# Optimization experiments

Hardware: AMD Instinct MI355X
Metric: run time of the kernel (lower is better)

The kernel has to match this reference:

```python
import jax, jax.numpy as jnp
import numpy as np

NUM_ROUTE = 3

def squash(x, axis=-1):
    sn = jnp.sum(x * x, axis=axis, keepdims=True)
    return (sn / (1.0 + sn)) * x / (jnp.sqrt(sn) + 1e-8)

def setup_inputs() -> dict:
    key = jax.random.key(0)
    ks = jax.random.split(key, 10)
    B, T, N, D = 16, 12, 1024, 64
    E, ES, HS, HT = 16, 16, 16, 64
    TT = HS * T
    u = lambda k, sh: jax.random.uniform(k, sh, jnp.float32, -0.1, 0.1)
    return {
        "x": jax.random.normal(ks[0], (B, T, N, D), jnp.float32),
        "node_embeddings": jax.random.normal(ks[1], (N, E), jnp.float32),
        "time_eb": jax.random.normal(ks[2], (B, ES), jnp.float32),
        "teb": jax.random.normal(ks[3], (B, T, ES), jnp.float32),
        "W_p": u(ks[4], (D, D)),
        "b_p": u(ks[5], (D,)),
        "t_adj": u(ks[6], (ES, HT, TT)),
        "adj": u(ks[7], (ES, HS, N)),
        "weights_spa": u(ks[8], (E, D, D)),
        "bias_spa": u(ks[9], (E, D)),
    }

def reference(x, node_embeddings, time_eb, teb, W_p, b_p, t_adj, adj, weights_spa, bias_spa):
    B, T, N, D = x.shape
    HS = adj.shape[1]
    lrelu = lambda y: jax.nn.leaky_relu(y, 0.01)

    # primary capsules
    Pcaps_out = squash(x @ W_p.T + b_p)                      # [B,T,N,D]
    dadj = jnp.einsum('btd,dhn->bthn', teb, adj)             # [B,T,HS,N]
    test1 = jnp.einsum('bthn,btnd->bthd', jax.nn.softmax(dadj, axis=-2), Pcaps_out)

    # prediction tensor u_hat[b,t,h,n,d] = squash(test1)[b,t,h,d] * Pcaps_out[b,t,n,d]
    k_test = jax.lax.stop_gradient(Pcaps_out)
    u_hat = jax.lax.stop_gradient(squash(test1)[:, :, :, None, :] * Pcaps_out[:, :, None, :, :])

    # dynamic routing-by-agreement (detached, as in the torch code)
    b = jnp.zeros((B, T, HS, N), x.dtype)
    for _ in range(NUM_ROUTE):
        c = jax.nn.softmax(b, axis=2)
        v = squash(jnp.einsum('bthn,bthnd->bthd', c, u_hat))
        b = b + jnp.einsum('bthd,btnd->bthn', v, k_test)

    c = jax.nn.softmax(b + dadj, axis=2)                     # [B,T,HS,N]
    s = jnp.einsum('bthn,btnd->bthd', c, Pcaps_out)          # [B,T,HS,D]

    mask_template = jnp.linspace(1.0, float(T), T) / 12.0    # [T]
    hyper = (s + mask_template[None, :, None, None]).reshape(B, T * HS, D)

    dyn = jnp.einsum('bd,dhk->bhk', time_eb, t_adj)          # [B,HT,TT]
    tem = lrelu(jnp.einsum('bhk,bkd->bhd', dyn, hyper))      # [B,HT,D]
    ret = lrelu(jnp.einsum('bhk,bhd->bkd', dyn, tem)).reshape(B, T, HS, D) + s

    v2 = squash(ret)
    recon = jnp.einsum('bthn,bthd->btnd', c, v2)             # [B,T,N,D]

    w_sp = jnp.einsum('nd,dio->nio', node_embeddings, weights_spa)  # [N,D,D]
    b_sp = node_embeddings @ bias_spa                                # [N,D]
    out = jnp.einsum('btni,nio->btno', recon, w_sp) + b_sp
    return lrelu(out + x), jax.lax.stop_gradient(c), jax.lax.stop_gradient(dyn)
```

## Files before the change

### kernel.cpp

```cpp
#include <hip/hip_runtime.h>
#include <math.h>

#define B_ 16
#define T_ 12
#define N_ 1024
#define D_ 64
#define HS_ 16
#define HT_ 64
#define TT_ 192
#define BT_ 192

typedef _Float16 f16x2 __attribute__((ext_vector_type(2)));
typedef _Float16 f16x8v __attribute__((ext_vector_type(8)));
typedef float f32x4v __attribute__((ext_vector_type(4)));
typedef unsigned int u32x4v __attribute__((ext_vector_type(4)));

__device__ __forceinline__ unsigned int pkrtz(float a, float b){
    auto r = __builtin_amdgcn_cvt_pkrtz(a, b);
    return __builtin_bit_cast(unsigned int, r);
}
__device__ __forceinline__ float fdot2u(unsigned int a, unsigned int b, float c){
    return __builtin_amdgcn_fdot2(__builtin_bit_cast(f16x2, a),
                                  __builtin_bit_cast(f16x2, b), c, false);
}
__device__ __forceinline__ float loF(unsigned int a){ f16x2 h = __builtin_bit_cast(f16x2, a); return (float)h.x; }
__device__ __forceinline__ float hiF(unsigned int a){ f16x2 h = __builtin_bit_cast(f16x2, a); return (float)h.y; }

__device__ __forceinline__ float lrelu_(float v){ return v > 0.f ? v : 0.01f*v; }
__device__ __forceinline__ float squash_sc(float sn){ return (sn/(1.f+sn))/(sqrtf(sn)+1e-8f); }

__device__ __forceinline__ float wredsum64(float v){
    #pragma unroll
    for (int mk = 1; mk < 64; mk <<= 1) v += __shfl_xor(v, mk, 64);
    return v;
}

__global__ __launch_bounds__(256, 1) void k_P(const float* __restrict__ x,
        const float* __restrict__ Wp, const float* __restrict__ bp,
        unsigned int* __restrict__ Ppk){
    __shared__ unsigned int xst[128*36];
    int t = threadIdx.x, w = t >> 6, l = t & 63;
    int lr = l & 15, lk = l >> 4;
    size_t rbase = (size_t)blockIdx.x*1024 + blockIdx.y*128;
    const float* xb = x + rbase*64;
    #pragma unroll
    for (int j = 0; j < 16; ++j){
        int idx = j*256 + t;
        int row = idx >> 5, cp = idx & 31;
        float2 xv = *(const float2*)(xb + row*64 + 2*cp);
        xst[row*36 + cp] = pkrtz(xv.x, xv.y);
    }
    f16x8v bf[4][2];
    float bpv[4];
    #pragma unroll
    for (int nt = 0; nt < 4; ++nt){
        #pragma unroll
        for (int ks = 0; ks < 2; ++ks){
            const float* wr = Wp + (nt*16 + lr)*64 + ks*32 + lk*8;
            u32x4v bw;
            #pragma unroll
            for (int j = 0; j < 4; ++j){
                float2 w2 = *(const float2*)(wr + 2*j);
                bw[j] = pkrtz(w2.x, w2.y);
            }
            bf[nt][ks] = __builtin_bit_cast(f16x8v, bw);
        }
        bpv[nt] = bp[nt*16 + lr];
    }
    __syncthreads();

    #pragma unroll
    for (int mi = 0; mi < 2; ++mi){
        int mt = 2*w + mi;
        f32x4v acc0 = {0.f,0.f,0.f,0.f}, acc1 = {0.f,0.f,0.f,0.f};
        f32x4v acc2 = {0.f,0.f,0.f,0.f}, acc3 = {0.f,0.f,0.f,0.f};
        #pragma unroll
        for (int ks = 0; ks < 2; ++ks){
            u32x4v au = *(u32x4v*)&xst[(mt*16 + lr)*36 + ks*16 + lk*4];
            f16x8v af = __builtin_bit_cast(f16x8v, au);
            acc0 = __builtin_amdgcn_mfma_f32_16x16x32_f16(af, bf[0][ks], acc0, 0, 0, 0);
            acc1 = __builtin_amdgcn_mfma_f32_16x16x32_f16(af, bf[1][ks], acc1, 0, 0, 0);
            acc2 = __builtin_amdgcn_mfma_f32_16x16x32_f16(af, bf[2][ks], acc2, 0, 0, 0);
            acc3 = __builtin_amdgcn_mfma_f32_16x16x32_f16(af, bf[3][ks], acc3, 0, 0, 0);
        }
        #pragma unroll
        for (int i = 0; i < 4; ++i){
            int row = mt*16 + lk*4 + i;
            float y0 = acc0[i] + bpv[0];
            float y1 = acc1[i] + bpv[1];
            float y2 = acc2[i] + bpv[2];
            float y3 = acc3[i] + bpv[3];
            float p0 = __shfl_xor(y0, 1, 64);
            float p1 = __shfl_xor(y1, 1, 64);
            float p2 = __shfl_xor(y2, 1, 64);
            float p3 = __shfl_xor(y3, 1, 64);
            if (!(l & 1)){
                int cb = lr >> 1;
                xst[row*36 +      cb] = pkrtz(y0, p0);
                xst[row*36 +  8 + cb] = pkrtz(y1, p1);
                xst[row*36 + 16 + cb] = pkrtz(y2, p2);
                xst[row*36 + 24 + cb] = pkrtz(y3, p3);
            }
        }
    }
    __syncthreads();
    unsigned int* pb = Ppk + rbase*32;
    #pragma unroll
    for (int q = 0; q < 4; ++q){
        int idx4 = q*256 + t;
        int r2 = idx4 >> 3, jq = idx4 & 7;
        uint4 v;
        v.x = xst[r2*36 + 4*jq];   v.y = xst[r2*36 + 4*jq + 1];
        v.z = xst[r2*36 + 4*jq+2]; v.w = xst[r2*36 + 4*jq + 3];
        ((uint4*)pb)[idx4] = v;
    }
}

template<int MODE>
__global__ __launch_bounds__(256, 2) void kA(const unsigned int* __restrict__ Ppk,
        float* __restrict__ scb,
        const float* __restrict__ teb, const float* __restrict__ adj,
        float* __restrict__ dadjb,
        const float* __restrict__ tpIn, const float* __restrict__ spart,
        float* __restrict__ v1buf, const float* __restrict__ vsumIn,
        float* __restrict__ vsumOut,
        float* __restrict__ tpOut, float* __restrict__ spOut,
        float* __restrict__ cout){
    __shared__ unsigned int PL[128*36];
    __shared__ unsigned int vLp[16*36];
    __shared__ float bL[16*130];
    __shared__ float cL[128*20];
    __shared__ float scL[128];
    __shared__ float snH[2][128];
    int bt = blockIdx.x, ch = blockIdx.y;
    int t = threadIdx.x, w = t >> 6, l = t & 63;
    int n0 = ch*128;

    const uint4* Pg = (const uint4*)(Ppk + ((size_t)bt*1024 + n0)*32);
    #pragma unroll
    for (int k = 0; k < 4; ++k){
        int idx4 = t + 256*k;
        uint4 u = Pg[idx4];
        *(uint4*)&PL[(idx4 >> 3)*36 + 4*(idx4 & 7)] = u;
    }
    if (MODE != 0){
        if (t < 128) scL[t] = scb[(size_t)bt*1024 + n0 + t];
        float sp = 0.f;
        if (MODE == 1){
            #pragma unroll
            for (int c = 0; c < 8; ++c) sp += spart[((size_t)bt*8 + c)*64 + l];
            sp *= (1.f/16.f);
        }
        #pragma unroll
        for (int i = 0; i < 4; ++i){
            int h = 4*w + i;
            float s = 0.f;
            #pragma unroll
            for (int c = 0; c < 8; ++c)
                s += tpIn[(((size_t)bt*8 + c)*16 + h)*64 + l];
            size_t oi = ((size_t)bt*16 + h)*64 + l;
            float vs;
            if (MODE == 1){
                float sn = wredsum64(s*s);
                float v1 = s*squash_sc(sn);
                v1buf[oi] = v1;
                float q = v1*sp;
                float sn2 = wredsum64(q*q);
                vs = q*squash_sc(sn2);
            } else {
                float q = v1buf[oi]*s;
                float sn = wredsum64(q*q);
                vs = vsumIn[oi] + q*squash_sc(sn);
            }
            if (MODE != 3) vsumOut[oi] = vs;
            float vo = __shfl_xor(vs, 1, 64);
            if (!(l & 1)) vLp[h*36 + (l >> 1)] = pkrtz(vs, vo);
        }
    }
    __syncthreads();

    {
        int n = t & 127, hg = t >> 7;
        if (MODE == 0){
            float s = 0.f;
            #pragma unroll
            for (int j = 0; j < 4; ++j){
                uint4 pq = *(uint4*)&PL[n*36 + hg*16 + 4*j];
                s += loF(pq.x)*loF(pq.x) + hiF(pq.x)*hiF(pq.x);
                s += loF(pq.y)*loF(pq.y) + hiF(pq.y)*hiF(pq.y);
                s += loF(pq.z)*loF(pq.z) + hiF(pq.z)*hiF(pq.z);
                s += loF(pq.w)*loF(pq.w) + hiF(pq.w)*hiF(pq.w);
            }
            snH[hg][n] = s;
        }
        float acc8[8];
        #pragma unroll
        for (int i = 0; i < 8; ++i) acc8[i] = 0.f;
        if (MODE != 0){
            #pragma unroll
            for (int j = 0; j < 8; ++j){
                uint4 pq = *(uint4*)&PL[n*36 + 4*j];
                #pragma unroll
                for (int i = 0; i < 8; ++i){
                    uint4 vq = *(uint4*)&vLp[(hg*8 + i)*36 + 4*j];
                    acc8[i] = fdot2u(pq.x, vq.x, acc8[i]);
                    acc8[i] = fdot2u(pq.y, vq.y, acc8[i]);
                    acc8[i] = fdot2u(pq.z, vq.z, acc8[i]);
                    acc8[i] = fdot2u(pq.w, vq.w, acc8[i]);
                }
            }
            float scn = scL[n];
            #pragma unroll
            for (int i = 0; i < 8; ++i) acc8[i] *= scn;
        }
        if (MODE == 0){
            float tl[16];
            #pragma unroll
            for (int e = 0; e < 16; ++e) tl[e] = teb[bt*16 + e];
            #pragma unroll
            for (int i = 0; i < 8; ++i){
                int h = hg*8 + i;
                float s = 0.f;
                #pragma unroll
                for (int e = 0; e < 16; ++e)
                    s += tl[e]*adj[(((e << 4) + h) << 10) + n0 + n];
                acc8[i] = s;
                dadjb[((size_t)bt*16 + h)*1024 + n0 + n] = s;
            }
        }
        if (MODE == 3){
            #pragma unroll
            for (int i = 0; i < 8; ++i)
                acc8[i] += dadjb[((size_t)bt*16 + hg*8 + i)*1024 + n0 + n];
        }
        #pragma unroll
        for (int i = 0; i < 8; ++i) bL[(hg*8 + i)*130 + n] = acc8[i];
    }
    __syncthreads();

    if (t < 128){
        int n = t;
        float scn;
        if (MODE == 0){
            scn = squash_sc(snH[0][n] + snH[1][n]);
            scL[n] = scn;
            scb[(size_t)bt*1024 + n0 + n] = scn;
        } else {
            scn = scL[n];
        }
        float M = -1e30f;
        #pragma unroll
        for (int h = 0; h < 16; ++h) M = fmaxf(M, bL[h*130 + n]);
        float S = 0.f; float ev[16];
        #pragma unroll
        for (int h = 0; h < 16; ++h){ ev[h] = __expf(bL[h*130 + n] - M); S += ev[h]; }
        float inv = 1.f/S;
        #pragma unroll
        for (int h = 0; h < 16; ++h){
            float cv = ev[h]*inv;
            cL[n*20 + h] = cv*scn;
            if (MODE == 3) cout[((size_t)bt*16 + h)*1024 + n0 + n] = cv;
        }
    }
    __syncthreads();

    float acc[4] = {0.f,0.f,0.f,0.f};
    float sp2 = 0.f;
    #pragma unroll 2
    for (int n = 0; n < 128; ++n){
        unsigned int pv = PL[n*36 + (l >> 1)];
        float p = (l & 1) ? hiF(pv) : loF(pv);
        float4 c4 = *(float4*)&cL[n*20 + 4*w];
        acc[0] += c4.x*p; acc[1] += c4.y*p; acc[2] += c4.z*p; acc[3] += c4.w*p;
        if (MODE == 0) sp2 += scL[n]*p;
    }
    #pragma unroll
    for (int i = 0; i < 4; ++i)
        tpOut[(((size_t)bt*8 + ch)*16 + 4*w + i)*64 + l] = acc[i];
    if (MODE == 0 && w == 0)
        spOut[((size_t)bt*8 + ch)*64 + l] = sp2;
}

__global__ __launch_bounds__(256) void k_s(const float* __restrict__ tpart,
        float* __restrict__ sout){
    int bt = blockIdx.x;
    int w = threadIdx.x >> 6, l = threadIdx.x & 63;
    #pragma unroll
    for (int i = 0; i < 4; ++i){
        int h = 4*w + i;
        float s = 0.f;
        #pragma unroll
        for (int c = 0; c < 8; ++c)
            s += tpart[(((size_t)bt*8 + c)*16 + h)*64 + l];
        sout[((size_t)bt*16 + h)*64 + l] = s;
    }
}

__global__ __launch_bounds__(256) void k_wsp(const float* __restrict__ ne,
        const float* __restrict__ wspa, const float* __restrict__ bspa,
        unsigned int* __restrict__ wpkg, float* __restrict__ bspg){
    __shared__ float wspaL[16*512];
    __shared__ float neL[32*16];
    int ioc = blockIdx.x, nc = blockIdx.y;
    int t = threadIdx.x, w = t >> 6, o = t & 63;
    #pragma unroll
    for (int k = 0; k < 8; ++k){
        int idx4 = t + 256*k;
        int e = idx4 >> 7, j4 = idx4 & 127;
        *(float4*)&wspaL[e*512 + 4*j4] =
            *(const float4*)(wspa + (size_t)e*4096 + ioc*512 + 4*j4);
    }
    #pragma unroll
    for (int k = 0; k < 2; ++k)
        neL[k*256 + t] = ne[(size_t)nc*512 + k*256 + t];
    __syncthreads();
    int c0 = (2*w)*64 + o, c1 = (2*w+1)*64 + o;
    #pragma unroll 2
    for (int n = 0; n < 32; ++n){
        float a0 = 0.f, a1 = 0.f;
        #pragma unroll
        for (int e = 0; e < 16; ++e){
            float nv = neL[n*16 + e];
            a0 += nv*wspaL[e*512 + c0];
            a1 += nv*wspaL[e*512 + c1];
        }
        wpkg[((size_t)(nc*32 + n))*2048 + (ioc*4 + w)*64 + o] = pkrtz(a0, a1);
    }
    if (ioc == 0){
        #pragma unroll
        for (int k = 0; k < 8; ++k){
            int idx = k*256 + t;
            int n = idx >> 6, o2 = idx & 63;
            float a = 0.f;
            #pragma unroll
            for (int e = 0; e < 16; ++e)
                a += neL[n*16 + e]*bspa[e*64 + o2];
            bspg[(size_t)(nc*32 + n)*64 + o2] = a;
        }
    }
}

__global__ __launch_bounds__(256) void k_dyntem(const float* __restrict__ timeb,
        const float* __restrict__ tadj, const float* __restrict__ sbuf,
        float* __restrict__ dyn, float* __restrict__ tem){
    __shared__ float dynL[192];
    __shared__ float part[4][64];
    int b = blockIdx.x, h = blockIdx.y, t = threadIdx.x;
    if (t < 192){
        float a = 0.f;
        #pragma unroll
        for (int e = 0; e < 16; ++e)
            a += timeb[b*16 + e]*tadj[((size_t)e*HT_ + h)*TT_ + t];
        dynL[t] = a;
        dyn[((size_t)b*HT_ + h)*TT_ + t] = a;
    }
    __syncthreads();
    int p = t >> 6, d = t & 63;
    const float* sb = sbuf + (size_t)b*TT_*64;
    float a = 0.f;
    #pragma unroll 4
    for (int k = 48*p; k < 48*p + 48; ++k)
        a += dynL[k]*(sb[(size_t)k*64 + d] + (float)((k >> 4) + 1)*(1.f/12.f));
    part[p][d] = a;
    __syncthreads();
    if (t < 64)
        tem[((size_t)b*HT_ + h)*64 + t] =
            lrelu_(part[0][t] + part[1][t] + part[2][t] + part[3][t]);
}

__global__ __launch_bounds__(256) void k_retv2(const float* __restrict__ dyn,
        const float* __restrict__ temb, const float* __restrict__ sbuf,
        float* __restrict__ v2){
    int b = blockIdx.x, kg = blockIdx.y;
    int w = threadIdx.x >> 6, l = threadIdx.x & 63;
    int k = kg*4 + w;
    const float* tb = temb + (size_t)b*HT_*64;
    float a0 = 0.f, a1 = 0.f;
    #pragma unroll 4
    for (int h = 0; h < HT_; h += 2){
        a0 += dyn[((size_t)b*HT_ + h  )*TT_ + k] * tb[(size_t)h*64 + l];
        a1 += dyn[((size_t)b*HT_ + h+1)*TT_ + k] * tb[(size_t)(h+1)*64 + l];
    }
    float a = lrelu_(a0 + a1);
    float r = a + sbuf[((size_t)b*TT_ + k)*64 + l];
    float sn = wredsum64(r*r);
    v2[((size_t)b*TT_ + k)*64 + l] = r*squash_sc(sn);
}

__global__ __launch_bounds__(256) void k_rec(const float* __restrict__ cbuf,
        const float* __restrict__ v2, unsigned int* __restrict__ recpk){
    __shared__ float vL[16*68];
    __shared__ float cL[16*132];
    int bt = blockIdx.x, nc = blockIdx.y;
    int t = threadIdx.x, l = t & 63, g = t >> 6;
    #pragma unroll
    for (int i = 0; i < 4; ++i){
        int idx = i*256 + t;
        vL[(idx>>6)*68 + (idx&63)] = v2[(size_t)bt*1024 + idx];
    }
    #pragma unroll
    for (int i = 0; i < 8; ++i){
        int idx = i*256 + t;
        cL[(idx>>7)*132 + (idx&127)] =
            cbuf[((size_t)bt*16 + (idx>>7))*1024 + nc*128 + (idx&127)];
    }
    __syncthreads();
    float vreg[16];
    #pragma unroll
    for (int h = 0; h < 16; ++h) vreg[h] = vL[h*68 + l];
    #pragma unroll 4
    for (int i = 0; i < 32; ++i){
        int nl = g + 4*i;
        float a = 0.f;
        #pragma unroll
        for (int h = 0; h < 16; ++h) a += cL[h*132 + nl]*vreg[h];
        float ap = __shfl_xor(a, 1, 64);
        if (!(l & 1))
            recpk[((size_t)(nc*128 + nl)*192 + bt)*32 + (l>>1)] = pkrtz(a, ap);
    }
}

__global__ __launch_bounds__(256) void k_final(const float* __restrict__ x,
        const unsigned int* __restrict__ wpkg, const float* __restrict__ bspg,
        const unsigned int* __restrict__ recpk, float* __restrict__ out){
    __shared__ __align__(16) unsigned int recL[96*32];
    int n = blockIdx.x, half = blockIdx.y;
    int t = threadIdx.x, l = t & 63, g = t >> 6;
    unsigned int wr[32];
    const unsigned int* wn = wpkg + (size_t)n*2048;
    #pragma unroll
    for (int ip = 0; ip < 32; ++ip) wr[ip] = wn[ip*64 + l];
    float bsp = bspg[(size_t)n*64 + l];
    {
        const uint4* src = (const uint4*)(recpk + ((size_t)n*192 + half*96)*32);
        #pragma unroll
        for (int k = 0; k < 3; ++k)
            ((uint4*)recL)[t + 256*k] = src[t + 256*k];
    }
    __syncthreads();
    #pragma unroll 2
    for (int i = 0; i < 24; ++i){
        int r = i*4 + g;
        int bt = half*96 + r;
        const uint4* rp = (const uint4*)&recL[r*32];
        float o0 = bsp, o1 = 0.f;
        #pragma unroll
        for (int jj = 0; jj < 8; ++jj){
            uint4 rq = rp[jj];
            o0 = fdot2u(rq.x, wr[4*jj+0], o0);
            o1 = fdot2u(rq.y, wr[4*jj+1], o1);
            o0 = fdot2u(rq.z, wr[4*jj+2], o0);
            o1 = fdot2u(rq.w, wr[4*jj+3], o1);
        }
        size_t oidx = ((size_t)bt*1024 + n)*64 + l;
        out[oidx] = lrelu_(o0 + o1 + x[oidx]);
    }
}

extern "C" void kernel_launch(void* const* d_in, const int* in_sizes, int n_in,
                              void* d_out, int out_size, void* d_ws, size_t ws_size,
                              hipStream_t stream) {
    const float* x     = (const float*)d_in[0];
    const float* ne    = (const float*)d_in[1];
    const float* timeb = (const float*)d_in[2];
    const float* teb   = (const float*)d_in[3];
    const float* Wp    = (const float*)d_in[4];
    const float* bp    = (const float*)d_in[5];
    const float* tadj  = (const float*)d_in[6];
    const float* adj   = (const float*)d_in[7];
    const float* wspa  = (const float*)d_in[8];
    const float* bspa  = (const float*)d_in[9];

    float* out    = (float*)d_out;
    float* outc   = out  + (size_t)BT_*N_*64;
    float* outdyn = outc + (size_t)BT_*HS_*N_;

    char* ws = (char*)d_ws;
    unsigned int* Ppk  = (unsigned int*)ws;
    float* dadj  = (float*)(ws + 25165824);
    float* tpA   = dadj  + (size_t)BT_*HS_*N_;
    float* tpB   = tpA   + (size_t)BT_*8*HS_*64;
    float* spart = tpB   + (size_t)BT_*8*HS_*64;
    float* v1buf = spart + (size_t)BT_*8*64;
    float* vs0   = v1buf + (size_t)BT_*HS_*64;
    float* vs1   = vs0   + (size_t)BT_*HS_*64;
    float* sbuf  = vs1   + (size_t)BT_*HS_*64;
    float* temb  = sbuf  + (size_t)BT_*HS_*64;
    float* v2    = temb  + (size_t)B_*HT_*64;
    unsigned int* recpk = (unsigned int*)(v2 + (size_t)BT_*HS_*64);
    float* scb = (float*)(recpk + (size_t)N_*BT_*32);
    unsigned int* wpkg = (unsigned int*)dadj;
    float* bspg = (float*)(wpkg + (size_t)N_*2048);

    k_P<<<dim3(BT_, 8), 256, 0, stream>>>(x, Wp, bp, Ppk);

    kA<0><<<dim3(BT_, 8), 256, 0, stream>>>(Ppk, scb, teb, adj, dadj, nullptr,
            nullptr, nullptr, nullptr, nullptr, tpA, spart, nullptr);
    kA<1><<<dim3(BT_, 8), 256, 0, stream>>>(Ppk, scb, teb, adj, dadj, tpA,
            spart, v1buf, nullptr, vs0, tpB, nullptr, nullptr);
    kA<2><<<dim3(BT_, 8), 256, 0, stream>>>(Ppk, scb, teb, adj, dadj, tpB,
            nullptr, v1buf, vs0, vs1, tpA, nullptr, nullptr);
    kA<3><<<dim3(BT_, 8), 256, 0, stream>>>(Ppk, scb, teb, adj, dadj, tpA,
            nullptr, v1buf, vs1, nullptr, tpB, nullptr, outc);
    k_s<<<dim3(BT_), 256, 0, stream>>>(tpB, sbuf);

    k_wsp<<<dim3(8, 32), 256, 0, stream>>>(ne, wspa, bspa, wpkg, bspg);

    k_dyntem<<<dim3(B_, HT_), 256, 0, stream>>>(timeb, tadj, sbuf, outdyn, temb);
    k_retv2<<<dim3(B_, 48), 256, 0, stream>>>(outdyn, temb, sbuf, v2);
    k_rec<<<dim3(BT_, 8), 256, 0, stream>>>(outc, v2, recpk);
    k_final<<<dim3(N_, 2), 256, 0, stream>>>(x, wpkg, bspg, recpk, out);
}
```

Measured before the change: 198.4 us.

## Use MFMA for routing logits and weighted capsule sums in kA

Replaces the fdot2-based routing logit computation (P·v) and the scalar c·P reduction in kA with 16x16x32 f16 MFMA instructions. To do this it builds a transposed packed copy of the P tile in shared memory and packs c·scale into f16 pairs. The goal is to cut the VALU cost of both inner products. In exchange it adds shuffle and transpose work during the load, more LDS use, and f16 rounding of the routing coefficients.

After: 176.2 us. 11.2% less time.

```diff
diff --git a/kernel.cpp b/kernel.cpp
--- a/kernel.cpp
+++ b/kernel.cpp
@@ -25,6 +25,10 @@
 }
 __device__ __forceinline__ float loF(unsigned int a){ f16x2 h = __builtin_bit_cast(f16x2, a); return (float)h.x; }
 __device__ __forceinline__ float hiF(unsigned int a){ f16x2 h = __builtin_bit_cast(f16x2, a); return (float)h.y; }
+__device__ __forceinline__ f32x4v mfma16(u32x4v a, u32x4v b, f32x4v c){
+    return __builtin_amdgcn_mfma_f32_16x16x32_f16(
+        __builtin_bit_cast(f16x8v, a), __builtin_bit_cast(f16x8v, b), c, 0, 0, 0);
+}
 
 __device__ __forceinline__ float lrelu_(float v){ return v > 0.f ? v : 0.01f*v; }
 __device__ __forceinline__ float squash_sc(float sn){ return (sn/(1.f+sn))/(sqrtf(sn)+1e-8f); }
@@ -127,13 +131,16 @@
         float* __restrict__ tpOut, float* __restrict__ spOut,
         float* __restrict__ cout){
     __shared__ unsigned int PL[128*36];
+    __shared__ unsigned int PLT[64*68];
     __shared__ unsigned int vLp[16*36];
     __shared__ float bL[16*130];
-    __shared__ float cL[128*20];
+    __shared__ unsigned int cpk[16*68];
     __shared__ float scL[128];
+    __shared__ unsigned int scpk[64];
     __shared__ float snH[2][128];
     int bt = blockIdx.x, ch = blockIdx.y;
     int t = threadIdx.x, w = t >> 6, l = t & 63;
+    int lr = l & 15, lk = l >> 4;
     int n0 = ch*128;
 
     const uint4* Pg = (const uint4*)(Ppk + ((size_t)bt*1024 + n0)*32);
@@ -141,7 +148,23 @@
     for (int k = 0; k < 4; ++k){
         int idx4 = t + 256*k;
         uint4 u = Pg[idx4];
-        *(uint4*)&PL[(idx4 >> 3)*36 + 4*(idx4 & 7)] = u;
+        int nn = idx4 >> 3, jq = idx4 & 7;
+        *(uint4*)&PL[nn*36 + 4*jq] = u;
+        unsigned int px = __shfl_xor(u.x, 8, 64);
+        unsigned int py = __shfl_xor(u.y, 8, 64);
+        unsigned int pz = __shfl_xor(u.z, 8, 64);
+        unsigned int pw = __shfl_xor(u.w, 8, 64);
+        if (!(nn & 1)){
+            int np = nn >> 1, d0 = jq*8;
+            PLT[(d0+0)*68 + np] = (u.x & 0xFFFFu) | (px << 16);
+            PLT[(d0+1)*68 + np] = (u.x >> 16)     | (px & 0xFFFF0000u);
+            PLT[(d0+2)*68 + np] = (u.y & 0xFFFFu) | (py << 16);
+            PLT[(d0+3)*68 + np] = (u.y >> 16)     | (py & 0xFFFF0000u);
+            PLT[(d0+4)*68 + np] = (u.z & 0xFFFFu) | (pz << 16);
+            PLT[(d0+5)*68 + np] = (u.z >> 16)     | (pz & 0xFFFF0000u);
+            PLT[(d0+6)*68 + np] = (u.w & 0xFFFFu) | (pw << 16);
+            PLT[(d0+7)*68 + np] = (u.w >> 16)     | (pw & 0xFFFF0000u);
+        }
     }
     if (MODE != 0){
         if (t < 128) scL[t] = scb[(size_t)bt*1024 + n0 + t];
@@ -179,106 +202,111 @@
     }
     __syncthreads();
 
-    {
-        int n = t & 127, hg = t >> 7;
-        if (MODE == 0){
+    if (MODE != 0){
+        #pragma unroll
+        for (int mi = 0; mi < 2; ++mi){
+            int mt = 2*w + mi;
+            f32x4v acc = {0.f,0.f,0.f,0.f};
+            #pragma unroll
+            for (int ks = 0; ks < 2; ++ks){
+                u32x4v au = *(u32x4v*)&PL[(mt*16 + lr)*36 + ks*16 + lk*4];
+                u32x4v bu = *(u32x4v*)&vLp[lr*36 + ks*16 + lk*4];
+                acc = mfma16(au, bu, acc);
+            }
+            #pragma unroll
+            for (int i = 0; i < 4; ++i){
+                int nn = mt*16 + lk*4 + i;
+                float lg = acc[i] * scL[nn];
+                if (MODE == 3)
+                    lg += dadjb[((size_t)bt*16 + lr)*1024 + n0 + nn];
+                bL[lr*130 + nn] = lg;
+            }
+        }
+    } else {
+        int nn = t & 127, hg = t >> 7;
+        float s2 = 0.f;
+        #pragma unroll
+        for (int j = 0; j < 4; ++j){
+            uint4 pq = *(uint4*)&PL[nn*36 + hg*16 + 4*j];
+            s2 += loF(pq.x)*loF(pq.x) + hiF(pq.x)*hiF(pq.x);
+            s2 += loF(pq.y)*loF(pq.y) + hiF(pq.y)*hiF(pq.y);
+            s2 += loF(pq.z)*loF(pq.z) + hiF(pq.z)*hiF(pq.z);
+            s2 += loF(pq.w)*loF(pq.w) + hiF(pq.w)*hiF(pq.w);
+        }
+        snH[hg][nn] = s2;
+        float tl[16];
+        #pragma unroll
+        for (int e = 0; e < 16; ++e) tl[e] = teb[bt*16 + e];
+        #pragma unroll
+        for (int i = 0; i < 8; ++i){
+            int h = hg*8 + i;
             float s = 0.f;
             #pragma unroll
-            for (int j = 0; j < 4; ++j){
-                uint4 pq = *(uint4*)&PL[n*36 + hg*16 + 4*j];
-                s += loF(pq.x)*loF(pq.x) + hiF(pq.x)*hiF(pq.x);
-                s += loF(pq.y)*loF(pq.y) + hiF(pq.y)*hiF(pq.y);
-                s += loF(pq.z)*loF(pq.z) + hiF(pq.z)*hiF(pq.z);
-                s += loF(pq.w)*loF(pq.w) + hiF(pq.w)*hiF(pq.w);
-            }
-            snH[hg][n] = s;
-        }
-        float acc8[8];
-        #pragma unroll
-        for (int i = 0; i < 8; ++i) acc8[i] = 0.f;
-        if (MODE != 0){
-            #pragma unroll
-            for (int j = 0; j < 8; ++j){
-                uint4 pq = *(uint4*)&PL[n*36 + 4*j];
-                #pragma unroll
-                for (int i = 0; i < 8; ++i){
-                    uint4 vq = *(uint4*)&vLp[(hg*8 + i)*36 + 4*j];
-                    acc8[i] = fdot2u(pq.x, vq.x, acc8[i]);
-                    acc8[i] = fdot2u(pq.y, vq.y, acc8[i]);
-                    acc8[i] = fdot2u(pq.z, vq.z, acc8[i]);
-                    acc8[i] = fdot2u(pq.w, vq.w, acc8[i]);
-                }
-            }
-            float scn = scL[n];
-            #pragma unroll
-            for (int i = 0; i < 8; ++i) acc8[i] *= scn;
-        }
-        if (MODE == 0){
-            float tl[16];
-            #pragma unroll
-            for (int e = 0; e < 16; ++e) tl[e] = teb[bt*16 + e];
-            #pragma unroll
-            for (int i = 0; i < 8; ++i){
-                int h = hg*8 + i;
-                float s = 0.f;
-                #pragma unroll
-                for (int e = 0; e < 16; ++e)
-                    s += tl[e]*adj[(((e << 4) + h) << 10) + n0 + n];
-                acc8[i] = s;
-                dadjb[((size_t)bt*16 + h)*1024 + n0 + n] = s;
-            }
-        }
-        if (MODE == 3){
-            #pragma unroll
-            for (int i = 0; i < 8; ++i)
-                acc8[i] += dadjb[((size_t)bt*16 + hg*8 + i)*1024 + n0 + n];
-        }
-        #pragma unroll
-        for (int i = 0; i < 8; ++i) bL[(hg*8 + i)*130 + n] = acc8[i];
+            for (int e = 0; e < 16; ++e)
+                s += tl[e]*adj[(((e << 4) + h) << 10) + n0 + nn];
+            bL[h*130 + nn] = s;
+            dadjb[((size_t)bt*16 + h)*1024 + n0 + nn] = s;
+        }
     }
     __syncthreads();
 
     if (t < 128){
-        int n = t;
+        int nn = t;
         float scn;
         if (MODE == 0){
-            scn = squash_sc(snH[0][n] + snH[1][n]);
-            scL[n] = scn;
-            scb[(size_t)bt*1024 + n0 + n] = scn;
+            scn = squash_sc(snH[0][nn] + snH[1][nn]);
+            scL[nn] = scn;
+            scb[(size_t)bt*1024 + n0 + nn] = scn;
+            float so = __shfl_xor(scn, 1, 64);
+            if (!(nn & 1)) scpk[nn >> 1] = pkrtz(scn, so);
         } else {
-            scn = scL[n];
+            scn = scL[nn];
         }
         float M = -1e30f;
         #pragma unroll
-        for (int h = 0; h < 16; ++h) M = fmaxf(M, bL[h*130 + n]);
+        for (int h = 0; h < 16; ++h) M = fmaxf(M, bL[h*130 + nn]);
         float S = 0.f; float ev[16];
         #pragma unroll
-        for (int h = 0; h < 16; ++h){ ev[h] = __expf(bL[h*130 + n] - M); S += ev[h]; }
+        for (int h = 0; h < 16; ++h){ ev[h] = __expf(bL[h*130 + nn] - M); S += ev[h]; }
         float inv = 1.f/S;
         #pragma unroll
         for (int h = 0; h < 16; ++h){
             float cv = ev[h]*inv;
-            cL[n*20 + h] = cv*scn;
-            if (MODE == 3) cout[((size_t)bt*16 + h)*1024 + n0 + n] = cv;
-        }
-    }
-    __syncthreads();
-
-    float acc[4] = {0.f,0.f,0.f,0.f};
-    float sp2 = 0.f;
-    #pragma unroll 2
-    for (int n = 0; n < 128; ++n){
-        unsigned int pv = PL[n*36 + (l >> 1)];
-        float p = (l & 1) ? hiF(pv) : loF(pv);
-        float4 c4 = *(float4*)&cL[n*20 + 4*w];
-        acc[0] += c4.x*p; acc[1] += c4.y*p; acc[2] += c4.z*p; acc[3] += c4.w*p;
-        if (MODE == 0) sp2 += scL[n]*p;
-    }
-    #pragma unroll
-    for (int i = 0; i < 4; ++i)
-        tpOut[(((size_t)bt*8 + ch)*16 + 4*w + i)*64 + l] = acc[i];
-    if (MODE == 0 && w == 0)
+            if (MODE == 3) cout[((size_t)bt*16 + h)*1024 + n0 + nn] = cv;
+            float cs = cv*scn;
+            float co = __shfl_xor(cs, 1, 64);
+            if (!(nn & 1)) cpk[h*68 + (nn >> 1)] = pkrtz(cs, co);
+        }
+    }
+    __syncthreads();
+
+    {
+        f32x4v acc = {0.f,0.f,0.f,0.f};
+        #pragma unroll
+        for (int ks = 0; ks < 4; ++ks){
+            u32x4v au = *(u32x4v*)&cpk[lr*68 + ks*16 + lk*4];
+            u32x4v bu = *(u32x4v*)&PLT[(w*16 + lr)*68 + ks*16 + lk*4];
+            acc = mfma16(au, bu, acc);
+        }
+        #pragma unroll
+        for (int i = 0; i < 4; ++i){
+            int h = lk*4 + i;
+            tpOut[(((size_t)bt*8 + ch)*16 + h)*64 + w*16 + lr] = acc[i];
+        }
+    }
+    if (MODE == 0 && w == 0){
+        float sp2 = 0.f;
+        #pragma unroll
+        for (int np4 = 0; np4 < 16; ++np4){
+            uint4 pq = *(uint4*)&PLT[l*68 + 4*np4];
+            uint4 sq = *(uint4*)&scpk[4*np4];
+            sp2 = fdot2u(pq.x, sq.x, sp2);
+            sp2 = fdot2u(pq.y, sq.y, sp2);
+            sp2 = fdot2u(pq.z, sq.z, sp2);
+            sp2 = fdot2u(pq.w, sq.w, sp2);
+        }
         spOut[((size_t)bt*8 + ch)*64 + l] = sp2;
+    }
 }
 
 __global__ __launch_bounds__(256) void k_s(const float* __restrict__ tpart,
```
